# Optimization experiments

Hardware: AMD Instinct MI355X
Metric: run time of the kernel (lower is better)

## Reference

```python
import jax, jax.numpy as jnp
import numpy as np

DIM = 1024
NUM_HEADS = 16
HEAD_DIM = DIM // NUM_HEADS
EPS = 1e-6


def _rmsnorm(x, w):
    # x: [B,H,N,D], w: [D]
    var = jnp.mean(x * x, axis=-1, keepdims=True)
    return x * jax.lax.rsqrt(var + EPS) * w


def _rotary(x, cos, sin):
    # x: [B,H,N,D]; cos/sin: [1,1,N,D/2]; complex-pair rotation (llama style)
    x2 = x.reshape(*x.shape[:-1], HEAD_DIM // 2, 2)
    xr, xi = x2[..., 0], x2[..., 1]
    or_ = xr * cos - xi * sin
    oi_ = xr * sin + xi * cos
    return jnp.stack([or_, oi_], axis=-1).reshape(x.shape)


def setup_inputs() -> dict:
    key = jax.random.key(0)
    ks = jax.random.split(key, 6)
    B, N = 2, 2048
    x = jax.random.normal(ks[0], (B, N, DIM), dtype=jnp.float32)
    pos = jax.random.uniform(ks[1], (N, HEAD_DIM // 2), dtype=jnp.float32)  # rotary angles
    s_in = 1.0 / np.sqrt(DIM)
    qkv_w = jax.random.normal(ks[2], (3 * DIM, DIM), dtype=jnp.float32) * s_in
    q_norm_w = jnp.ones((HEAD_DIM,), dtype=jnp.float32)
    k_norm_w = jnp.ones((HEAD_DIM,), dtype=jnp.float32)
    proj_w = jax.random.normal(ks[3], (DIM, DIM), dtype=jnp.float32) * s_in
    proj_b = jnp.zeros((DIM,), dtype=jnp.float32)
    return {"x": x, "pos": pos, "qkv_w": qkv_w, "q_norm_w": q_norm_w,
            "k_norm_w": k_norm_w, "proj_w": proj_w, "proj_b": proj_b}


def reference(x, pos, qkv_w, q_norm_w, k_norm_w, proj_w, proj_b):
    B, N, C = x.shape
    H, D = NUM_HEADS, HEAD_DIM
    scale = D ** -0.5
    # QKV projection: [B,N,3C] -> [3,B,H,N,D]
    qkv = jnp.einsum('bnc,fc->bnf', x, qkv_w)
    qkv = qkv.reshape(B, N, 3, H, D).transpose(2, 0, 3, 1, 4)
    q, k, v = qkv[0], qkv[1], qkv[2]
    # QK RMSNorm over head_dim
    q = _rmsnorm(q, q_norm_w)
    k = _rmsnorm(k, k_norm_w)
    # Rotary embedding (freqs_cis = exp(i * pos))
    cos = jnp.cos(pos)[None, None, :, :]
    sin = jnp.sin(pos)[None, None, :, :]
    q = _rotary(q, cos, sin)
    k = _rotary(k, cos, sin)
    # Scaled dot-product attention (non-causal)
    scores = jnp.einsum('bhnd,bhmd->bhnm', q, k) * scale
    attn = jax.nn.softmax(scores, axis=-1)
    out = jnp.einsum('bhnm,bhmd->bhnd', attn, v)
    out = out.transpose(0, 2, 1, 3).reshape(B, N, C)
    return jnp.einsum('bnc,oc->bno', out, proj_w) + proj_b
```

## Files before the change

### kernel.cpp

```cpp
#include <hip/hip_runtime.h>
#include <hip/hip_bf16.h>

typedef unsigned short ushort_t;
using floatx4 = __attribute__((__ext_vector_type__(4))) float;
using bf16x8  = __attribute__((__ext_vector_type__(8))) __bf16;
using ushort4v = __attribute__((__ext_vector_type__(4))) ushort_t;

__device__ __forceinline__ ushort_t f2bf(float f) {
  unsigned int u = __builtin_bit_cast(unsigned int, f);
  u += 0x7FFFu + ((u >> 16) & 1u);
  return (ushort_t)(u >> 16);
}
__device__ __forceinline__ float b2f(ushort_t h) {
  unsigned int u = ((unsigned int)h) << 16;
  return __builtin_bit_cast(float, u);
}
__device__ __forceinline__ unsigned int pkbf(float a, float b) {
  __hip_bfloat162 h = __float22bfloat162_rn(make_float2(a, b));
  unsigned int u;
  __builtin_memcpy(&u, &h, 4);
  return u;
}

__device__ __forceinline__ void gl2lds16(const ushort_t* g, ushort_t* l) {
  __builtin_amdgcn_global_load_lds(
      (const __attribute__((address_space(1))) unsigned int*)g,
      (__attribute__((address_space(3))) unsigned int*)l, 16, 0, 0);
}

__global__ void cast_all(const float* __restrict__ x, const float* __restrict__ qw,
                         const float* __restrict__ pw, ushort_t* __restrict__ ob) {
  const int T1 = 4096 * 1024, T2 = T1 + 3072 * 1024, T3 = T2 + 1024 * 1024;
  int i = (blockIdx.x * blockDim.x + threadIdx.x) * 4;
  if (i >= T3) return;
  const float* src = (i < T1) ? (x + i) : (i < T2) ? (qw + (i - T1)) : (pw + (i - T2));
  float4 v = *reinterpret_cast<const float4*>(src);
  uint2 o = make_uint2(pkbf(v.x, v.y), pkbf(v.z, v.w));
  *reinterpret_cast<uint2*>(&ob[i]) = o;
}

__global__ __launch_bounds__(256)
void gemm_qkv_fused(const ushort_t* __restrict__ A, const ushort_t* __restrict__ B,
                    const float* __restrict__ pos,
                    const float* __restrict__ qnw, const float* __restrict__ knw,
                    ushort_t* __restrict__ qr, ushort_t* __restrict__ kr,
                    ushort_t* __restrict__ vt) {
  const int K = 1024;
  __shared__ ushort_t sA[128 * 32];
  __shared__ ushort_t sB[128 * 32];
  __shared__ __align__(16) ushort_t sE[4][4096];
  const int m0 = blockIdx.y * 128, n0 = blockIdx.x * 128;
  const int tid = threadIdx.x;
  const int lane = tid & 63, w = tid >> 6;
  const int wm = (w >> 1) * 64;
  const int grp = lane >> 4, l16 = lane & 15;
  const int r0 = lane >> 2, c0 = (lane & 3) * 8;
  floatx4 acc[4][4] = {};
  for (int k0 = 0; k0 < K; k0 += 32) {
    __syncthreads();
#pragma unroll
    for (int i = 0; i < 2; i++) {
      const int j = w * 2 + i;
      gl2lds16(&A[(size_t)(m0 + j * 16 + r0) * K + k0 + c0], &sA[j * 512]);
      gl2lds16(&B[(size_t)(n0 + j * 16 + r0) * K + k0 + c0], &sB[j * 512]);
    }
    __syncthreads();
    bf16x8 af[4], bfr[4];
#pragma unroll
    for (int i = 0; i < 4; i++)
      af[i] = *reinterpret_cast<const bf16x8*>(&sA[(wm + i * 16 + l16) * 32 + grp * 8]);
#pragma unroll
    for (int i = 0; i < 4; i++)
      bfr[i] = *reinterpret_cast<const bf16x8*>(&sB[((w & 1) * 64 + i * 16 + l16) * 32 + grp * 8]);
#pragma unroll
    for (int i = 0; i < 4; i++)
#pragma unroll
      for (int j = 0; j < 4; j++)
        acc[i][j] = __builtin_amdgcn_mfma_f32_16x16x32_bf16(af[i], bfr[j], acc[i][j], 0, 0, 0);
  }
  const int region = n0 >> 10;
  const int h = ((n0 & 1023) >> 6) + (w & 1);
  const int tbase = m0 + wm;
  const int bb = tbase >> 11;
  const int nwin = tbase & 2047;
  const int q = lane & 7;
  const int lr = lane >> 3;

  if (region < 2) {
    float* sEf = (float*)&sE[w][0];
    const float* nwp = (region == 0) ? qnw : knw;
    const float qmul = (region == 0) ? 0.125f * 1.44269504088896340736f : 1.0f;
    float wgt[8];
    *(float4*)&wgt[0] = *(const float4*)&nwp[q * 8];
    *(float4*)&wgt[4] = *(const float4*)&nwp[q * 8 + 4];
#pragma unroll
    for (int hf = 0; hf < 2; hf++) {
      __syncthreads();
#pragma unroll
      for (int i2 = 0; i2 < 2; i2++)
#pragma unroll
        for (int rr = 0; rr < 4; rr++) {
          const int t2 = i2 * 16 + grp * 4 + rr;
#pragma unroll
          for (int j = 0; j < 4; j++) {
            const int cd = (j * 4 + (l16 >> 2)) ^ (t2 & 15);
            sEf[t2 * 64 + cd * 4 + (l16 & 3)] = acc[hf * 2 + i2][j][rr];
          }
        }
      __syncthreads();
#pragma unroll
      for (int tg = 0; tg < 4; tg++) {
        const int t2 = tg * 8 + lr;
        const int n = (tbase + hf * 32 + t2) & 2047;
        float v0[8];
        const int ck1 = (2 * q) ^ (t2 & 15), ck2 = (2 * q + 1) ^ (t2 & 15);
        *(float4*)&v0[0] = *(const float4*)&sEf[t2 * 64 + ck1 * 4];
        *(float4*)&v0[4] = *(const float4*)&sEf[t2 * 64 + ck2 * 4];
        float ss = 0.f;
#pragma unroll
        for (int e = 0; e < 8; e++) ss += v0[e] * v0[e];
        ss += __shfl_xor(ss, 1); ss += __shfl_xor(ss, 2); ss += __shfl_xor(ss, 4);
        const float rn = rsqrtf(ss * (1.0f / 64.0f) + 1e-6f);
        float4 ang = *(const float4*)&pos[n * 32 + q * 4];
        union { unsigned int u32[4]; uint4 v4; } ov;
#pragma unroll
        for (int p = 0; p < 4; p++) {
          const float a = ((const float*)&ang)[p];
          const float cc = __cosf(a), sn = __sinf(a);
          const float xr = v0[2 * p] * rn * wgt[2 * p];
          const float xi = v0[2 * p + 1] * rn * wgt[2 * p + 1];
          ov.u32[p] = pkbf((xr * cc - xi * sn) * qmul, (xr * sn + xi * cc) * qmul);
        }
        const size_t rowb = ((size_t)(bb * 16 + h) * 2048 + n) * 64;
        if (region == 0)
          *reinterpret_cast<uint4*>(&qr[rowb + q * 8]) = ov.v4;
        else
          *reinterpret_cast<uint4*>(&kr[rowb + (q ^ (n & 7)) * 8]) = ov.v4;
      }
    }
  } else {
    __syncthreads();
#pragma unroll
    for (int i = 0; i < 4; i++)
#pragma unroll
      for (int j = 0; j < 4; j++) {
        const int d = j * 16 + l16;
        const int ct = (i * 4 + grp) ^ (d & 15);
        uint2 pk = make_uint2(pkbf(acc[i][j][0], acc[i][j][1]),
                              pkbf(acc[i][j][2], acc[i][j][3]));
        *reinterpret_cast<uint2*>(&sE[w][d * 64 + ct * 4]) = pk;
      }
    __syncthreads();
#pragma unroll
    for (int dd = 0; dd < 8; dd++) {
      const int d = dd * 8 + lr;
      const int cta = 8 * (q >> 2) + (q & 3);
      union { ushort4v h[2]; uint4 v4; } ob;
      ob.h[0] = *reinterpret_cast<const ushort4v*>(&sE[w][d * 64 + ((cta ^ (d & 15)) * 4)]);
      ob.h[1] = *reinterpret_cast<const ushort4v*>(&sE[w][d * 64 + (((cta + 4) ^ (d & 15)) * 4)]);
      *reinterpret_cast<uint4*>(
          &vt[((size_t)(bb * 16 + h) * 64 + d) * 2048 + nwin + (q ^ (d & 7)) * 8]) = ob.v4;
    }
  }
}

__global__ __launch_bounds__(256)
void flash_attn(const ushort_t* __restrict__ qr, const ushort_t* __restrict__ kr,
                const ushort_t* __restrict__ vt, ushort_t* __restrict__ aout) {
  const int bh = blockIdx.y;
  const int w = threadIdx.x >> 6, lane = threadIdx.x & 63;
  const int grp = lane >> 4, l16 = lane & 15;
  const int sw = l16 & 7;
  const int q0 = blockIdx.x * 128 + w * 32;
  const size_t hb = (size_t)bh * 2048 * 64;

  __shared__ ushort_t sK[2][64 * 64];
  __shared__ ushort_t sV[2][64 * 64];

  bf16x8 qa[2][2];
#pragma unroll
  for (int f = 0; f < 2; f++) {
    const ushort_t* qp = &qr[hb + (size_t)(q0 + f * 16 + l16) * 64 + grp * 8];
    qa[f][0] = *reinterpret_cast<const bf16x8*>(qp);
    qa[f][1] = *reinterpret_cast<const bf16x8*>(qp + 32);
  }

  floatx4 o[2][4] = {};
  float l[2] = {0.f, 0.f};

  auto stage = [&](int buf, int k0) {
    const ushort_t* kg = &kr[hb + (size_t)k0 * 64];
#pragma unroll
    for (int i = 0; i < 2; i++) {
      const int j = w * 2 + i;
      gl2lds16(kg + j * 512 + lane * 8, &sK[buf][j * 512]);
    }
#pragma unroll
    for (int i = 0; i < 2; i++) {
      const int d = w * 16 + i * 8;
      gl2lds16(&vt[((size_t)bh * 64 + d + (lane >> 3)) * 2048 + k0 + (lane & 7) * 8],
               &sV[buf][d * 64]);
    }
  };

  stage(0, 0);
  const int g0 = (grp ^ sw) * 8;
  for (int it = 0; it < 32; it++) {
    const int cur = it & 1;
    __syncthreads();
    if (it + 1 < 32) stage(1 - cur, (it + 1) * 64);
    const ushort_t* kb = &sK[cur][0];
    const ushort_t* vb = &sV[cur][0];
    floatx4 s[2][4];
#pragma unroll
    for (int nt = 0; nt < 4; nt++) {
      const ushort_t* kp = kb + (nt * 16 + l16) * 64;
      bf16x8 kf0 = *reinterpret_cast<const bf16x8*>(kp + g0);
      bf16x8 kf1 = *reinterpret_cast<const bf16x8*>(kp + (g0 ^ 32));
#pragma unroll
      for (int f = 0; f < 2; f++) {
        floatx4 acc = {};
        acc = __builtin_amdgcn_mfma_f32_16x16x32_bf16(kf0, qa[f][0], acc, 0, 0, 0);
        acc = __builtin_amdgcn_mfma_f32_16x16x32_bf16(kf1, qa[f][1], acc, 0, 0, 0);
        s[f][nt] = acc;
      }
    }
    union { unsigned int u32[4]; bf16x8 v; } pf[2][2];
#pragma unroll
    for (int f = 0; f < 2; f++) {
      float p[4][4];
      float rs = 0.f;
#pragma unroll
      for (int nt = 0; nt < 4; nt++)
#pragma unroll
        for (int r = 0; r < 4; r++) {
          float pv = __builtin_amdgcn_exp2f(s[f][nt][r]);
          p[nt][r] = pv;
          rs += pv;
        }
      l[f] += rs;
#pragma unroll
      for (int c = 0; c < 2; c++) {
        pf[f][c].u32[0] = pkbf(p[2 * c][0], p[2 * c][1]);
        pf[f][c].u32[1] = pkbf(p[2 * c][2], p[2 * c][3]);
        pf[f][c].u32[2] = pkbf(p[2 * c + 1][0], p[2 * c + 1][1]);
        pf[f][c].u32[3] = pkbf(p[2 * c + 1][2], p[2 * c + 1][3]);
      }
    }
#pragma unroll
    for (int c = 0; c < 2; c++) {
#pragma unroll
      for (int dt = 0; dt < 4; dt++) {
        const bf16x8 vv = *reinterpret_cast<const bf16x8*>(
            vb + (dt * 16 + l16) * 64 + (((c * 4 + grp) ^ sw) << 3));
#pragma unroll
        for (int f = 0; f < 2; f++)
          o[f][dt] = __builtin_amdgcn_mfma_f32_16x16x32_bf16(vv, pf[f][c].v, o[f][dt], 0, 0, 0);
      }
    }
  }
  const int b = bh >> 4, h = bh & 15;
#pragma unroll
  for (int f = 0; f < 2; f++) {
    float lt = l[f] + __shfl_xor(l[f], 16);
    lt += __shfl_xor(lt, 32);
    const float rl = 1.0f / lt;
    const size_t orow = (size_t)(b * 2048 + q0 + f * 16 + l16) * 1024 + h * 64;
#pragma unroll
    for (int dt = 0; dt < 4; dt++) {
      uint2 ov = make_uint2(pkbf(o[f][dt][0] * rl, o[f][dt][1] * rl),
                            pkbf(o[f][dt][2] * rl, o[f][dt][3] * rl));
      *reinterpret_cast<uint2*>(&aout[orow + dt * 16 + grp * 4]) = ov;
    }
  }
}

__global__ __launch_bounds__(256)
void gemm_proj(const ushort_t* __restrict__ A, const ushort_t* __restrict__ B,
               float* __restrict__ Cout, const float* __restrict__ bias) {
  const int K = 1024, N = 1024;
  __shared__ ushort_t sA[128 * 32];
  __shared__ ushort_t sB[64 * 32];
  const int m0 = blockIdx.y * 128, n0 = blockIdx.x * 64;
  const int tid = threadIdx.x;
  const int lane = tid & 63, w = tid >> 6;
  const int wm = (w >> 1) * 64, wn = (w & 1) * 32;
  const int grp = lane >> 4, l16 = lane & 15;
  const int r0 = lane >> 2, c0 = (lane & 3) * 8;
  floatx4 acc[4][2] = {};
  for (int k0 = 0; k0 < K; k0 += 32) {
    __syncthreads();
#pragma unroll
    for (int i = 0; i < 2; i++) {
      const int j = w * 2 + i;
      gl2lds16(&A[(size_t)(m0 + j * 16 + r0) * K + k0 + c0], &sA[j * 512]);
    }
    gl2lds16(&B[(size_t)(n0 + w * 16 + r0) * K + k0 + c0], &sB[w * 512]);
    __syncthreads();
    bf16x8 af[4], bfr[2];
#pragma unroll
    for (int i = 0; i < 4; i++)
      af[i] = *reinterpret_cast<const bf16x8*>(&sA[(wm + i * 16 + l16) * 32 + grp * 8]);
#pragma unroll
    for (int j = 0; j < 2; j++)
      bfr[j] = *reinterpret_cast<const bf16x8*>(&sB[(wn + j * 16 + l16) * 32 + grp * 8]);
#pragma unroll
    for (int i = 0; i < 4; i++)
#pragma unroll
      for (int j = 0; j < 2; j++)
        acc[i][j] = __builtin_amdgcn_mfma_f32_16x16x32_bf16(af[i], bfr[j], acc[i][j], 0, 0, 0);
  }
#pragma unroll
  for (int i = 0; i < 4; i++) {
    const int mb = m0 + wm + i * 16 + grp * 4;
#pragma unroll
    for (int j = 0; j < 2; j++) {
      const int nc = n0 + wn + j * 16 + l16;
      const float bv = bias[nc];
#pragma unroll
      for (int rr = 0; rr < 4; rr++)
        Cout[(size_t)(mb + rr) * N + nc] = acc[i][j][rr] + bv;
    }
  }
}

extern "C" void kernel_launch(void* const* d_in, const int* in_sizes, int n_in,
                              void* d_out, int out_size, void* d_ws, size_t ws_size,
                              hipStream_t stream) {
  const float* x      = (const float*)d_in[0];
  const float* pos    = (const float*)d_in[1];
  const float* qkv_w  = (const float*)d_in[2];
  const float* q_nw   = (const float*)d_in[3];
  const float* k_nw   = (const float*)d_in[4];
  const float* proj_w = (const float*)d_in[5];
  const float* proj_b = (const float*)d_in[6];
  float* out = (float*)d_out;

  ushort_t* x_b     = (ushort_t*)d_ws;
  ushort_t* qkvw_b  = x_b     + (size_t)4096 * 1024;
  ushort_t* projw_b = qkvw_b  + (size_t)3072 * 1024;
  ushort_t* q_r     = projw_b + (size_t)1024 * 1024;
  ushort_t* k_r     = q_r     + (size_t)32 * 2048 * 64;
  ushort_t* v_t     = k_r     + (size_t)32 * 2048 * 64;
  ushort_t* a_out   = v_t     + (size_t)32 * 2048 * 64;

  cast_all<<<8388608 / 4 / 256, 256, 0, stream>>>(x, qkv_w, proj_w, x_b);

  gemm_qkv_fused<<<dim3(3072 / 128, 4096 / 128), 256, 0, stream>>>(
      x_b, qkvw_b, pos, q_nw, k_nw, q_r, k_r, v_t);

  flash_attn<<<dim3(2048 / 128, 32), 256, 0, stream>>>(q_r, k_r, v_t, a_out);

  gemm_proj<<<dim3(1024 / 64, 4096 / 128), 256, 0, stream>>>(a_out, projw_b, out, proj_b);
}
```

Measured before the change: 217.6 us.

## Precompute rotary table, widen attention K tile, MFMA row-sum, staged proj stores

The cast kernel now also builds a cos/sin table from pos, so the QKV epilogue reads the table instead of evaluating trig functions. Flash attention stages 128 keys per iteration instead of 64, doubling LDS buffers and halving barriers. The softmax row sum is now computed with an extra MFMA against a vector of ones rather than with scalar adds and shuffles. The projection epilogue goes through LDS so the output is written as coalesced float4 stores. The larger LDS footprint may reduce occupancy, and the cos/sin table adds global memory traffic.

```diff
diff --git a/kernel.cpp b/kernel.cpp
--- a/kernel.cpp
+++ b/kernel.cpp
@@ -6,15 +6,6 @@
 using bf16x8  = __attribute__((__ext_vector_type__(8))) __bf16;
 using ushort4v = __attribute__((__ext_vector_type__(4))) ushort_t;
 
-__device__ __forceinline__ ushort_t f2bf(float f) {
-  unsigned int u = __builtin_bit_cast(unsigned int, f);
-  u += 0x7FFFu + ((u >> 16) & 1u);
-  return (ushort_t)(u >> 16);
-}
-__device__ __forceinline__ float b2f(ushort_t h) {
-  unsigned int u = ((unsigned int)h) << 16;
-  return __builtin_bit_cast(float, u);
-}
 __device__ __forceinline__ unsigned int pkbf(float a, float b) {
   __hip_bfloat162 h = __float22bfloat162_rn(make_float2(a, b));
   unsigned int u;
@@ -29,19 +20,27 @@
 }
 
 __global__ void cast_all(const float* __restrict__ x, const float* __restrict__ qw,
-                         const float* __restrict__ pw, ushort_t* __restrict__ ob) {
+                         const float* __restrict__ pw, ushort_t* __restrict__ ob,
+                         const float* __restrict__ pos, float* __restrict__ cs) {
   const int T1 = 4096 * 1024, T2 = T1 + 3072 * 1024, T3 = T2 + 1024 * 1024;
-  int i = (blockIdx.x * blockDim.x + threadIdx.x) * 4;
-  if (i >= T3) return;
-  const float* src = (i < T1) ? (x + i) : (i < T2) ? (qw + (i - T1)) : (pw + (i - T2));
-  float4 v = *reinterpret_cast<const float4*>(src);
-  uint2 o = make_uint2(pkbf(v.x, v.y), pkbf(v.z, v.w));
-  *reinterpret_cast<uint2*>(&ob[i]) = o;
+  const int tid = blockIdx.x * blockDim.x + threadIdx.x;
+  if (tid < 65536) {
+    const float a = pos[tid];
+    cs[2 * tid]     = __cosf(a);
+    cs[2 * tid + 1] = __sinf(a);
+  }
+  const int i = tid * 4;
+  if (i < T3) {
+    const float* src = (i < T1) ? (x + i) : (i < T2) ? (qw + (i - T1)) : (pw + (i - T2));
+    float4 v = *reinterpret_cast<const float4*>(src);
+    uint2 o = make_uint2(pkbf(v.x, v.y), pkbf(v.z, v.w));
+    *reinterpret_cast<uint2*>(&ob[i]) = o;
+  }
 }
 
 __global__ __launch_bounds__(256)
 void gemm_qkv_fused(const ushort_t* __restrict__ A, const ushort_t* __restrict__ B,
-                    const float* __restrict__ pos,
+                    const float* __restrict__ cs,
                     const float* __restrict__ qnw, const float* __restrict__ knw,
                     ushort_t* __restrict__ qr, ushort_t* __restrict__ kr,
                     ushort_t* __restrict__ vt) {
@@ -121,12 +120,14 @@
         for (int e = 0; e < 8; e++) ss += v0[e] * v0[e];
         ss += __shfl_xor(ss, 1); ss += __shfl_xor(ss, 2); ss += __shfl_xor(ss, 4);
         const float rn = rsqrtf(ss * (1.0f / 64.0f) + 1e-6f);
-        float4 ang = *(const float4*)&pos[n * 32 + q * 4];
+        float4 c01 = *(const float4*)&cs[(n * 32 + q * 4) * 2];
+        float4 c23 = *(const float4*)&cs[(n * 32 + q * 4) * 2 + 4];
+        float ccv[4] = {c01.x, c01.z, c23.x, c23.z};
+        float snv[4] = {c01.y, c01.w, c23.y, c23.w};
         union { unsigned int u32[4]; uint4 v4; } ov;
 #pragma unroll
         for (int p = 0; p < 4; p++) {
-          const float a = ((const float*)&ang)[p];
-          const float cc = __cosf(a), sn = __sinf(a);
+          const float cc = ccv[p], sn = snv[p];
           const float xr = v0[2 * p] * rn * wgt[2 * p];
           const float xi = v0[2 * p + 1] * rn * wgt[2 * p + 1];
           ov.u32[p] = pkbf((xr * cc - xi * sn) * qmul, (xr * sn + xi * cc) * qmul);
@@ -174,8 +175,8 @@
   const int q0 = blockIdx.x * 128 + w * 32;
   const size_t hb = (size_t)bh * 2048 * 64;
 
-  __shared__ ushort_t sK[2][64 * 64];
-  __shared__ ushort_t sV[2][64 * 64];
+  __shared__ ushort_t sK[2][128 * 64];
+  __shared__ ushort_t sV[2][64 * 128];
 
   bf16x8 qa[2][2];
 #pragma unroll
@@ -186,85 +187,88 @@
   }
 
   floatx4 o[2][4] = {};
-  float l[2] = {0.f, 0.f};
+  floatx4 ol[2] = {};
+
+  union { ushort_t u[8]; bf16x8 v; } onef;
+#pragma unroll
+  for (int e = 0; e < 8; e++) onef.u[e] = 0x3F80;
 
   auto stage = [&](int buf, int k0) {
     const ushort_t* kg = &kr[hb + (size_t)k0 * 64];
 #pragma unroll
-    for (int i = 0; i < 2; i++) {
-      const int j = w * 2 + i;
+    for (int i = 0; i < 4; i++) {
+      const int j = w * 4 + i;
       gl2lds16(kg + j * 512 + lane * 8, &sK[buf][j * 512]);
     }
 #pragma unroll
-    for (int i = 0; i < 2; i++) {
-      const int d = w * 16 + i * 8;
-      gl2lds16(&vt[((size_t)bh * 64 + d + (lane >> 3)) * 2048 + k0 + (lane & 7) * 8],
-               &sV[buf][d * 64]);
+    for (int i = 0; i < 4; i++) {
+      const int d = w * 16 + i * 4;
+      gl2lds16(&vt[((size_t)bh * 64 + d + (lane >> 4)) * 2048 + k0 + (lane & 15) * 8],
+               &sV[buf][d * 128]);
     }
   };
 
   stage(0, 0);
   const int g0 = (grp ^ sw) * 8;
-  for (int it = 0; it < 32; it++) {
+  for (int it = 0; it < 16; it++) {
     const int cur = it & 1;
     __syncthreads();
-    if (it + 1 < 32) stage(1 - cur, (it + 1) * 64);
-    const ushort_t* kb = &sK[cur][0];
-    const ushort_t* vb = &sV[cur][0];
-    floatx4 s[2][4];
-#pragma unroll
-    for (int nt = 0; nt < 4; nt++) {
-      const ushort_t* kp = kb + (nt * 16 + l16) * 64;
-      bf16x8 kf0 = *reinterpret_cast<const bf16x8*>(kp + g0);
-      bf16x8 kf1 = *reinterpret_cast<const bf16x8*>(kp + (g0 ^ 32));
+    if (it + 1 < 16) stage(1 - cur, (it + 1) * 128);
+#pragma unroll
+    for (int hh = 0; hh < 2; hh++) {
+      const ushort_t* kb = &sK[cur][hh * 64 * 64];
+      const ushort_t* vb = &sV[cur][hh * 64];
+      floatx4 s[2][4];
+#pragma unroll
+      for (int nt = 0; nt < 4; nt++) {
+        const ushort_t* kp = kb + (nt * 16 + l16) * 64;
+        bf16x8 kf0 = *reinterpret_cast<const bf16x8*>(kp + g0);
+        bf16x8 kf1 = *reinterpret_cast<const bf16x8*>(kp + (g0 ^ 32));
+#pragma unroll
+        for (int f = 0; f < 2; f++) {
+          floatx4 acc = {};
+          acc = __builtin_amdgcn_mfma_f32_16x16x32_bf16(kf0, qa[f][0], acc, 0, 0, 0);
+          acc = __builtin_amdgcn_mfma_f32_16x16x32_bf16(kf1, qa[f][1], acc, 0, 0, 0);
+          s[f][nt] = acc;
+        }
+      }
+      union { unsigned int u32[4]; bf16x8 v; } pf[2][2];
 #pragma unroll
       for (int f = 0; f < 2; f++) {
-        floatx4 acc = {};
-        acc = __builtin_amdgcn_mfma_f32_16x16x32_bf16(kf0, qa[f][0], acc, 0, 0, 0);
-        acc = __builtin_amdgcn_mfma_f32_16x16x32_bf16(kf1, qa[f][1], acc, 0, 0, 0);
-        s[f][nt] = acc;
-      }
-    }
-    union { unsigned int u32[4]; bf16x8 v; } pf[2][2];
-#pragma unroll
-    for (int f = 0; f < 2; f++) {
-      float p[4][4];
-      float rs = 0.f;
-#pragma unroll
-      for (int nt = 0; nt < 4; nt++)
-#pragma unroll
-        for (int r = 0; r < 4; r++) {
-          float pv = __builtin_amdgcn_exp2f(s[f][nt][r]);
-          p[nt][r] = pv;
-          rs += pv;
-        }
-      l[f] += rs;
+        float p[4][4];
+#pragma unroll
+        for (int nt = 0; nt < 4; nt++)
+#pragma unroll
+          for (int r = 0; r < 4; r++)
+            p[nt][r] = __builtin_amdgcn_exp2f(s[f][nt][r]);
+#pragma unroll
+        for (int c = 0; c < 2; c++) {
+          pf[f][c].u32[0] = pkbf(p[2 * c][0], p[2 * c][1]);
+          pf[f][c].u32[1] = pkbf(p[2 * c][2], p[2 * c][3]);
+          pf[f][c].u32[2] = pkbf(p[2 * c + 1][0], p[2 * c + 1][1]);
+          pf[f][c].u32[3] = pkbf(p[2 * c + 1][2], p[2 * c + 1][3]);
+        }
+      }
 #pragma unroll
       for (int c = 0; c < 2; c++) {
-        pf[f][c].u32[0] = pkbf(p[2 * c][0], p[2 * c][1]);
-        pf[f][c].u32[1] = pkbf(p[2 * c][2], p[2 * c][3]);
-        pf[f][c].u32[2] = pkbf(p[2 * c + 1][0], p[2 * c + 1][1]);
-        pf[f][c].u32[3] = pkbf(p[2 * c + 1][2], p[2 * c + 1][3]);
-      }
-    }
-#pragma unroll
-    for (int c = 0; c < 2; c++) {
-#pragma unroll
-      for (int dt = 0; dt < 4; dt++) {
-        const bf16x8 vv = *reinterpret_cast<const bf16x8*>(
-            vb + (dt * 16 + l16) * 64 + (((c * 4 + grp) ^ sw) << 3));
 #pragma unroll
         for (int f = 0; f < 2; f++)
-          o[f][dt] = __builtin_amdgcn_mfma_f32_16x16x32_bf16(vv, pf[f][c].v, o[f][dt], 0, 0, 0);
+          ol[f] = __builtin_amdgcn_mfma_f32_16x16x32_bf16(onef.v, pf[f][c].v, ol[f], 0, 0, 0);
+#pragma unroll
+        for (int dt = 0; dt < 4; dt++) {
+          const bf16x8 vv = *reinterpret_cast<const bf16x8*>(
+              vb + (dt * 16 + l16) * 128 + (((c * 4 + grp) ^ sw) << 3));
+#pragma unroll
+          for (int f = 0; f < 2; f++)
+            o[f][dt] = __builtin_amdgcn_mfma_f32_16x16x32_bf16(vv, pf[f][c].v, o[f][dt], 0, 0, 0);
+        }
       }
     }
   }
   const int b = bh >> 4, h = bh & 15;
 #pragma unroll
   for (int f = 0; f < 2; f++) {
-    float lt = l[f] + __shfl_xor(l[f], 16);
-    lt += __shfl_xor(lt, 32);
-    const float rl = 1.0f / lt;
+    const float rl = 1.0f / ol[f][0];
     const size_t orow = (size_t)(b * 2048 + q0 + f * 16 + l16) * 1024 + h * 64;
 #pragma unroll
     for (int dt = 0; dt < 4; dt++) {
@@ -281,6 +285,7 @@
   const int K = 1024, N = 1024;
   __shared__ ushort_t sA[128 * 32];
   __shared__ ushort_t sB[64 * 32];
+  __shared__ float sT[4][2048];
   const int m0 = blockIdx.y * 128, n0 = blockIdx.x * 64;
   const int tid = threadIdx.x;
   const int lane = tid & 63, w = tid >> 6;
@@ -310,17 +315,27 @@
       for (int j = 0; j < 2; j++)
         acc[i][j] = __builtin_amdgcn_mfma_f32_16x16x32_bf16(af[i], bfr[j], acc[i][j], 0, 0, 0);
   }
-#pragma unroll
-  for (int i = 0; i < 4; i++) {
-    const int mb = m0 + wm + i * 16 + grp * 4;
+  float bv[2];
+#pragma unroll
+  for (int j = 0; j < 2; j++) bv[j] = bias[n0 + wn + j * 16 + l16];
+#pragma unroll
+  for (int i = 0; i < 4; i++)
 #pragma unroll
     for (int j = 0; j < 2; j++) {
-      const int nc = n0 + wn + j * 16 + l16;
-      const float bv = bias[nc];
-#pragma unroll
-      for (int rr = 0; rr < 4; rr++)
-        Cout[(size_t)(mb + rr) * N + nc] = acc[i][j][rr] + bv;
-    }
+      const int col = j * 16 + l16, c4 = col >> 2;
+#pragma unroll
+      for (int rr = 0; rr < 4; rr++) {
+        const int row = i * 16 + grp * 4 + rr;
+        sT[w][row * 32 + ((c4 ^ (row & 7)) << 2) + (col & 3)] = acc[i][j][rr] + bv[j];
+      }
+    }
+  __builtin_amdgcn_s_waitcnt(0);
+  const int lr = lane >> 3, ch = lane & 7;
+#pragma unroll
+  for (int rg = 0; rg < 8; rg++) {
+    const int row = rg * 8 + lr;
+    float4 vvv = *(const float4*)&sT[w][row * 32 + ((ch ^ (row & 7)) << 2)];
+    *reinterpret_cast<float4*>(&Cout[(size_t)(m0 + wm + row) * N + n0 + wn + ch * 4]) = vvv;
   }
 }
 
@@ -343,11 +358,12 @@
   ushort_t* k_r     = q_r     + (size_t)32 * 2048 * 64;
   ushort_t* v_t     = k_r     + (size_t)32 * 2048 * 64;
   ushort_t* a_out   = v_t     + (size_t)32 * 2048 * 64;
-
-  cast_all<<<8388608 / 4 / 256, 256, 0, stream>>>(x, qkv_w, proj_w, x_b);
+  float*    cs_tab  = (float*)(a_out + (size_t)4096 * 1024);
+
+  cast_all<<<8388608 / 4 / 256, 256, 0, stream>>>(x, qkv_w, proj_w, x_b, pos, cs_tab);
 
   gemm_qkv_fused<<<dim3(3072 / 128, 4096 / 128), 256, 0, stream>>>(
-      x_b, qkvw_b, pos, q_nw, k_nw, q_r, k_r, v_t);
+      x_b, qkvw_b, cs_tab, q_nw, k_nw, q_r, k_r, v_t);
 
   flash_attn<<<dim3(2048 / 128, 32), 256, 0, stream>>>(q_r, k_r, v_t, a_out);
 
```

After: 214.3 us. No clear change (-1.5%).
